# Kernel optimization log

Measured on AMD Instinct MI355X. Metric: run time of the kernel, lower is better.

Reference implementation:

```python
import jax, jax.numpy as jnp
import numpy as np

N_NODES = 50000
N_GRAPHS = 64
HID = 128
IN_DIM = 128
N_LAYERS = 3


def setup_inputs() -> dict:
    key = jax.random.key(0)
    ks = jax.random.split(key, 12)
    x = jax.random.normal(ks[0], (N_NODES, IN_DIM), dtype=jnp.float32)
    edge_index = jax.random.randint(ks[1], (2, 800000), 0, N_NODES, dtype=jnp.int64)
    batch = jnp.sort(jax.random.randint(ks[2], (N_NODES,), 0, N_GRAPHS, dtype=jnp.int64))
    s = 1.0 / np.sqrt(HID)
    W0 = jax.random.normal(ks[3], (IN_DIM, HID), dtype=jnp.float32) * s
    b0 = jnp.zeros((HID,), dtype=jnp.float32)
    Ws = jax.random.normal(ks[4], (N_LAYERS, HID, HID), dtype=jnp.float32) * s
    bs = jnp.zeros((N_LAYERS, HID), dtype=jnp.float32)
    W1 = jax.random.normal(ks[5], (HID, HID // 2), dtype=jnp.float32) * s
    b1 = jnp.zeros((HID // 2,), dtype=jnp.float32)
    W2 = jax.random.normal(ks[6], (HID // 2, 2), dtype=jnp.float32) * (1.0 / np.sqrt(HID // 2))
    b2 = jnp.zeros((2,), dtype=jnp.float32)
    return {"x": x, "edge_index": edge_index, "batch": batch,
            "W0": W0, "b0": b0, "Ws": Ws, "bs": bs,
            "W1": W1, "b1": b1, "W2": W2, "b2": b2}


def reference(x, edge_index, batch, W0, b0, Ws, bs, W1, b1, W2, b2):
    n = x.shape[0]
    # GCN: add self-loops, symmetric normalization D^-1/2 (A+I) D^-1/2
    loop = jnp.arange(n, dtype=edge_index.dtype)
    src = jnp.concatenate([edge_index[0], loop])  # [E+N]
    dst = jnp.concatenate([edge_index[1], loop])
    deg = jax.ops.segment_sum(jnp.ones_like(dst, dtype=x.dtype), dst, num_segments=n)
    dinv = jax.lax.rsqrt(jnp.maximum(deg, 1.0))
    coef = (dinv[src] * dinv[dst])[:, None]  # [E+N, 1]

    def gcn(h, W, b):
        hw = h @ W                                  # transform first (cheaper)
        agg = jax.ops.segment_sum(hw[src] * coef, dst, num_segments=n)
        return jax.nn.relu(agg + b)

    h = gcn(x, W0, b0)
    for i in range(Ws.shape[0]):
        h = gcn(h, Ws[i], bs[i])

    # global mean pool over graphs
    sums = jax.ops.segment_sum(h, batch, num_segments=N_GRAPHS)
    cnts = jax.ops.segment_sum(jnp.ones((n,), dtype=h.dtype), batch, num_segments=N_GRAPHS)
    pooled = sums / jnp.maximum(cnts, 1.0)[:, None]  # [G, HID]

    out = jax.nn.relu(pooled @ W1 + b1) @ W2 + b2    # [G, 2]
    return out
```

## Files before the change

kernel.cpp:

```cpp
#include <hip/hip_runtime.h>
#include <hip/hip_bf16.h>
#include <hip/hip_fp16.h>

#define HID 128
#define N_GRAPHS 64

__global__ void init_deg_kernel(int* __restrict__ deg, int n) {
    int i = blockIdx.x * 256 + threadIdx.x;
    if (i < n) deg[i] = 1;
}

__global__ void count_kernel(const int* __restrict__ dst, int* __restrict__ deg, int E) {
    int e = blockIdx.x * 256 + threadIdx.x;
    if (e < E) atomicAdd(&deg[dst[e]], 1);
}

__global__ __launch_bounds__(256) void scan_partial_kernel(const int* __restrict__ deg,
                                                           int* __restrict__ bsum, int n) {
    __shared__ int red[256];
    int t = threadIdx.x;
    int i = blockIdx.x * 256 + t;
    red[t] = (i < n) ? deg[i] : 0;
    __syncthreads();
#pragma unroll
    for (int s = 128; s > 0; s >>= 1) {
        if (t < s) red[t] += red[t + s];
        __syncthreads();
    }
    if (t == 0) bsum[blockIdx.x] = red[0];
}

__global__ __launch_bounds__(256) void scan_bsum_kernel(const int* __restrict__ bsum,
                                                        int* __restrict__ boff,
                                                        int* __restrict__ row_ptr,
                                                        int nb, int n) {
    __shared__ int arr[256];
    int t = threadIdx.x;
    int own = (t < nb) ? bsum[t] : 0;
    arr[t] = own;
    __syncthreads();
#pragma unroll
    for (int off = 1; off < 256; off <<= 1) {
        int v = arr[t];
        int add = (t >= off) ? arr[t - off] : 0;
        __syncthreads();
        arr[t] = v + add;
        __syncthreads();
    }
    if (t < nb) boff[t] = arr[t] - own;
    if (t == 255) row_ptr[n] = arr[255];
}

__global__ __launch_bounds__(256) void scan_emit_kernel(const int* __restrict__ deg,
                                                        const int* __restrict__ boff,
                                                        int* __restrict__ row_ptr,
                                                        int* __restrict__ cursor,
                                                        float* __restrict__ dinv, int n) {
    __shared__ int arr[256];
    int t = threadIdx.x;
    int i = blockIdx.x * 256 + t;
    int d = (i < n) ? deg[i] : 0;
    arr[t] = d;
    __syncthreads();
#pragma unroll
    for (int off = 1; off < 256; off <<= 1) {
        int v = arr[t];
        int add = (t >= off) ? arr[t - off] : 0;
        __syncthreads();
        arr[t] = v + add;
        __syncthreads();
    }
    if (i < n) {
        int pos = boff[blockIdx.x] + arr[t] - d;
        row_ptr[i] = pos;
        cursor[i] = pos;
        dinv[i] = rsqrtf((float)d);
    }
}

__global__ void fill_kernel(const int* __restrict__ src, const int* __restrict__ dst,
                            int* __restrict__ cursor, int* __restrict__ col,
                            int E, int EN) {
    int e = blockIdx.x * 256 + threadIdx.x;
    if (e >= EN) return;
    int s, d;
    if (e < E) { s = src[e]; d = dst[e]; }
    else       { s = e - E; d = s; }
    int pos = atomicAdd(&cursor[d], 1);
    col[pos] = s;
}

__global__ __launch_bounds__(256, 2) void gemm_scale_kernel(const float* __restrict__ A,
                                                            const float* __restrict__ W,
                                                            const float* __restrict__ dinv,
                                                            __half* __restrict__ out16, int M) {
    __shared__ float sAT[32][132];
    __shared__ float sW[32][132];
    int tid = threadIdx.x;
    int row0 = blockIdx.x * 128;
    int ty = tid >> 4, tx = tid & 15;
    int r0 = ty * 8;
    int cl = tx * 4;
    int ch = 64 + tx * 4;

    float acc[8][8];
#pragma unroll
    for (int i = 0; i < 8; ++i)
#pragma unroll
        for (int j = 0; j < 8; ++j) acc[i][j] = 0.f;

    for (int kc = 0; kc < 128; kc += 32) {
#pragma unroll
        for (int p = 0; p < 4; ++p) {
            int idx = tid + p * 256;
            int k = idx >> 5, c4 = idx & 31;
            float4 v = *(const float4*)(W + (size_t)(kc + k) * 128 + c4 * 4);
            *(float4*)&sW[k][c4 * 4] = v;
        }
#pragma unroll
        for (int p = 0; p < 4; ++p) {
            int idx = tid + p * 256;
            int r = idx >> 3, c4 = idx & 7;
            float4 v = make_float4(0.f, 0.f, 0.f, 0.f);
            if (row0 + r < M) v = *(const float4*)(A + (size_t)(row0 + r) * 128 + kc + c4 * 4);
            sAT[c4 * 4 + 0][r] = v.x;
            sAT[c4 * 4 + 1][r] = v.y;
            sAT[c4 * 4 + 2][r] = v.z;
            sAT[c4 * 4 + 3][r] = v.w;
        }
        __syncthreads();

#pragma unroll 4
        for (int k = 0; k < 32; ++k) {
            float4 a0 = *(float4*)&sAT[k][r0];
            float4 a1 = *(float4*)&sAT[k][r0 + 4];
            float4 w0 = *(float4*)&sW[k][cl];
            float4 w1 = *(float4*)&sW[k][ch];
            float a[8] = {a0.x, a0.y, a0.z, a0.w, a1.x, a1.y, a1.z, a1.w};
            float w[8] = {w0.x, w0.y, w0.z, w0.w, w1.x, w1.y, w1.z, w1.w};
#pragma unroll
            for (int i = 0; i < 8; ++i)
#pragma unroll
                for (int j = 0; j < 8; ++j)
                    acc[i][j] += a[i] * w[j];
        }
        __syncthreads();
    }

#pragma unroll
    for (int i = 0; i < 8; ++i) {
        int r = row0 + r0 + i;
        if (r < M) {
            float dv = dinv[r];
            __half2 h0 = __floats2half2_rn(acc[i][0] * dv, acc[i][1] * dv);
            __half2 h1 = __floats2half2_rn(acc[i][2] * dv, acc[i][3] * dv);
            __half2 h2 = __floats2half2_rn(acc[i][4] * dv, acc[i][5] * dv);
            __half2 h3 = __floats2half2_rn(acc[i][6] * dv, acc[i][7] * dv);
            float2 plo, phi;
            ((__half2*)&plo)[0] = h0; ((__half2*)&plo)[1] = h1;
            ((__half2*)&phi)[0] = h2; ((__half2*)&phi)[1] = h3;
            *(float2*)(out16 + (size_t)r * 128 + cl) = plo;
            *(float2*)(out16 + (size_t)r * 128 + ch) = phi;
        }
    }
}

__global__ __launch_bounds__(256) void aggregate_kernel(const __half* __restrict__ hw,
                                                        const int* __restrict__ row_ptr,
                                                        const int* __restrict__ col,
                                                        const float* __restrict__ dinv,
                                                        const float* __restrict__ bias,
                                                        float* __restrict__ out, int n) {
    int tid = threadIdx.x;
    int v = blockIdx.x * 8 + (tid >> 5);
    if (v >= n) return;
    int j = (tid & 31) * 4;
    int p0 = row_ptr[v], p1 = row_ptr[v + 1];
    float4 acc = make_float4(0.f, 0.f, 0.f, 0.f);
    int p = p0;
    for (; p + 3 < p1; p += 4) {
        int s0 = col[p], s1 = col[p + 1], s2 = col[p + 2], s3 = col[p + 3];
        float2 r0 = *(const float2*)(hw + (size_t)s0 * 128 + j);
        float2 r1 = *(const float2*)(hw + (size_t)s1 * 128 + j);
        float2 r2 = *(const float2*)(hw + (size_t)s2 * 128 + j);
        float2 r3 = *(const float2*)(hw + (size_t)s3 * 128 + j);
        float2 a0 = __half22float2(((__half2*)&r0)[0]), a1 = __half22float2(((__half2*)&r0)[1]);
        float2 b0 = __half22float2(((__half2*)&r1)[0]), b1 = __half22float2(((__half2*)&r1)[1]);
        float2 c0 = __half22float2(((__half2*)&r2)[0]), c1 = __half22float2(((__half2*)&r2)[1]);
        float2 d0 = __half22float2(((__half2*)&r3)[0]), d1 = __half22float2(((__half2*)&r3)[1]);
        acc.x += (a0.x + b0.x) + (c0.x + d0.x);
        acc.y += (a0.y + b0.y) + (c0.y + d0.y);
        acc.z += (a1.x + b1.x) + (c1.x + d1.x);
        acc.w += (a1.y + b1.y) + (c1.y + d1.y);
    }
    for (; p < p1; ++p) {
        int s0 = col[p];
        float2 r0 = *(const float2*)(hw + (size_t)s0 * 128 + j);
        float2 a0 = __half22float2(((__half2*)&r0)[0]), a1 = __half22float2(((__half2*)&r0)[1]);
        acc.x += a0.x; acc.y += a0.y; acc.z += a1.x; acc.w += a1.y;
    }
    float dv = dinv[v];
    float4 bb = *(const float4*)(bias + j);
    float4 o;
    o.x = fmaxf(acc.x * dv + bb.x, 0.f);
    o.y = fmaxf(acc.y * dv + bb.y, 0.f);
    o.z = fmaxf(acc.z * dv + bb.z, 0.f);
    o.w = fmaxf(acc.w * dv + bb.w, 0.f);
    *(float4*)(out + (size_t)v * 128 + j) = o;
}

__global__ void boundary_kernel(const int* __restrict__ batch, int* __restrict__ start, int n) {
    int i = blockIdx.x * 256 + threadIdx.x;
    if (i >= n) return;
    int b = batch[i];
    int pb = (i > 0) ? batch[i - 1] : -1;
    if (b != pb) {
        for (int g = pb + 1; g <= b; ++g) start[g] = i;
    }
    if (i == n - 1) {
        for (int g = b + 1; g <= N_GRAPHS; ++g) start[g] = n;
    }
}

__global__ __launch_bounds__(256) void pool_reduce_kernel(const float* __restrict__ h,
                                                          const int* __restrict__ start,
                                                          float* __restrict__ pooled) {
    __shared__ float part[8][128];
    int g = blockIdx.x;
    int s = start[g], e = start[g + 1];
    int tid = threadIdx.x;
    int grp = tid >> 5;
    int j = (tid & 31) * 4;
    float4 acc = make_float4(0.f, 0.f, 0.f, 0.f);
    for (int v = s + grp; v < e; v += 8) {
        float4 a = *(const float4*)(h + (size_t)v * 128 + j);
        acc.x += a.x; acc.y += a.y; acc.z += a.z; acc.w += a.w;
    }
    *(float4*)&part[grp][j] = acc;
    __syncthreads();
    if (tid < 128) {
        float sum = 0.f;
#pragma unroll
        for (int k = 0; k < 8; ++k) sum += part[k][tid];
        int cntv = e - s; if (cntv < 1) cntv = 1;
        pooled[g * 128 + tid] = sum / (float)cntv;
    }
}

__global__ __launch_bounds__(256) void mlp_kernel(const float* __restrict__ pooled_g,
                                                  const float* __restrict__ W1,
                                                  const float* __restrict__ b1,
                                                  const float* __restrict__ W2,
                                                  const float* __restrict__ b2,
                                                  float* __restrict__ out) {
    __shared__ float pooled[64][128];
    __shared__ float h1[64][64];
    int tid = threadIdx.x;
    for (int i = tid; i < 64 * 128; i += 256) pooled[i >> 7][i & 127] = pooled_g[i];
    __syncthreads();
    for (int i = tid; i < 64 * 64; i += 256) {
        int g = i >> 6, j = i & 63;
        float acc = b1[j];
        for (int k = 0; k < 128; ++k) acc += pooled[g][k] * W1[k * 64 + j];
        h1[g][j] = fmaxf(acc, 0.f);
    }
    __syncthreads();
    if (tid < 128) {
        int g = tid >> 1, c = tid & 1;
        float acc = b2[c];
        for (int jj = 0; jj < 64; ++jj) acc += h1[g][jj] * W2[jj * 2 + c];
        out[tid] = acc;
    }
}

extern "C" void kernel_launch(void* const* d_in, const int* in_sizes, int n_in,
                              void* d_out, int out_size, void* d_ws, size_t ws_size,
                              hipStream_t stream) {
    const float* x    = (const float*)d_in[0];
    const int*   ei   = (const int*)d_in[1];
    const int*   batch= (const int*)d_in[2];
    const float* W0   = (const float*)d_in[3];
    const float* b0   = (const float*)d_in[4];
    const float* Ws   = (const float*)d_in[5];
    const float* bs   = (const float*)d_in[6];
    const float* W1   = (const float*)d_in[7];
    const float* b1   = (const float*)d_in[8];
    const float* W2   = (const float*)d_in[9];
    const float* b2   = (const float*)d_in[10];
    float* out = (float*)d_out;

    const int n  = in_sizes[0] / HID;
    const int E  = in_sizes[1] / 2;
    const int EN = E + n;
    const int* src = ei;
    const int* dst = ei + E;
    const int nb = (n + 255) / 256;

    char* ws = (char*)d_ws;
    size_t off = 0;
    auto alloc = [&](size_t bytes) { void* p = ws + off; off = (off + bytes + 255) & ~(size_t)255; return p; };
    float*  bufA   = (float*) alloc((size_t)n * HID * 4);
    __half* hw16   = (__half*)alloc((size_t)n * HID * 2);
    float*  dinv   = (float*) alloc((size_t)n * 4);
    int*    row_ptr= (int*)   alloc((size_t)(n + 1) * 4);
    int*    cursor = (int*)   alloc((size_t)n * 4);
    int*    deg    = (int*)   alloc((size_t)n * 4);
    int*    col    = (int*)   alloc((size_t)EN * 4);
    int*    bsum   = (int*)   alloc((size_t)nb * 4);
    int*    boff   = (int*)   alloc((size_t)nb * 4);
    int*    gstart = (int*)   alloc((N_GRAPHS + 1) * 4);
    float*  pooled = (float*) alloc(N_GRAPHS * 128 * 4);
    (void)ws_size; (void)n_in; (void)out_size;

    init_deg_kernel<<<nb, 256, 0, stream>>>(deg, n);
    count_kernel<<<(E + 255) / 256, 256, 0, stream>>>(dst, deg, E);
    scan_partial_kernel<<<nb, 256, 0, stream>>>(deg, bsum, n);
    scan_bsum_kernel<<<1, 256, 0, stream>>>(bsum, boff, row_ptr, nb, n);
    scan_emit_kernel<<<nb, 256, 0, stream>>>(deg, boff, row_ptr, cursor, dinv, n);
    fill_kernel<<<(EN + 255) / 256, 256, 0, stream>>>(src, dst, cursor, col, E, EN);
    boundary_kernel<<<nb, 256, 0, stream>>>(batch, gstart, n);

    const int gemm_grid = (n + 127) / 128;
    const int node_grid = (n + 7) / 8;

    gemm_scale_kernel<<<gemm_grid, 256, 0, stream>>>(x, W0, dinv, hw16, n);
    aggregate_kernel<<<node_grid, 256, 0, stream>>>(hw16, row_ptr, col, dinv, b0, bufA, n);
    for (int l = 0; l < 3; ++l) {
        gemm_scale_kernel<<<gemm_grid, 256, 0, stream>>>(bufA, Ws + (size_t)l * HID * HID, dinv, hw16, n);
        aggregate_kernel<<<node_grid, 256, 0, stream>>>(hw16, row_ptr, col, dinv, bs + (size_t)l * HID, bufA, n);
    }

    pool_reduce_kernel<<<N_GRAPHS, 256, 0, stream>>>(bufA, gstart, pooled);
    mlp_kernel<<<1, 256, 0, stream>>>(pooled, W1, b1, W2, b2, out);
}
```

Before: 509.6 us.

## Double-buffer GEMM tiles with smaller row blocks and widen aggregate gathers

The GEMM now handles 64 rows per block instead of 128, with each thread computing an 8x4 tile. It double-buffers the A and W shared-memory tiles, loading the next K chunk into registers while the current chunk is being computed. This gives more blocks and hides global-load latency, but halves per-thread register reuse of the W values. The aggregate kernel now uses 16 threads per node, each gathering 16-byte (8 half) chunks, so each edge row is fetched with fewer, wider loads.

```diff
diff --git a/kernel.cpp b/kernel.cpp
--- a/kernel.cpp
+++ b/kernel.cpp
@@ -90,61 +90,98 @@
     col[pos] = s;
 }
 
-__global__ __launch_bounds__(256, 2) void gemm_scale_kernel(const float* __restrict__ A,
-                                                            const float* __restrict__ W,
-                                                            const float* __restrict__ dinv,
-                                                            __half* __restrict__ out16, int M) {
-    __shared__ float sAT[32][132];
-    __shared__ float sW[32][132];
+__global__ __launch_bounds__(256) void gemm_scale_kernel(const float* __restrict__ A,
+                                                         const float* __restrict__ W,
+                                                         const float* __restrict__ dinv,
+                                                         __half* __restrict__ out16, int M) {
+    __shared__ float sAT[2][32][68];
+    __shared__ float sW [2][32][132];
     int tid = threadIdx.x;
-    int row0 = blockIdx.x * 128;
-    int ty = tid >> 4, tx = tid & 15;
+    int row0 = blockIdx.x * 64;
+    int ty = tid >> 5, tx = tid & 31;
     int r0 = ty * 8;
-    int cl = tx * 4;
-    int ch = 64 + tx * 4;
-
-    float acc[8][8];
+    int j0 = tx * 4;
+
+    float acc[8][4];
 #pragma unroll
     for (int i = 0; i < 8; ++i)
 #pragma unroll
-        for (int j = 0; j < 8; ++j) acc[i][j] = 0.f;
-
-    for (int kc = 0; kc < 128; kc += 32) {
-#pragma unroll
-        for (int p = 0; p < 4; ++p) {
-            int idx = tid + p * 256;
-            int k = idx >> 5, c4 = idx & 31;
-            float4 v = *(const float4*)(W + (size_t)(kc + k) * 128 + c4 * 4);
-            *(float4*)&sW[k][c4 * 4] = v;
-        }
-#pragma unroll
-        for (int p = 0; p < 4; ++p) {
-            int idx = tid + p * 256;
-            int r = idx >> 3, c4 = idx & 7;
-            float4 v = make_float4(0.f, 0.f, 0.f, 0.f);
-            if (row0 + r < M) v = *(const float4*)(A + (size_t)(row0 + r) * 128 + kc + c4 * 4);
-            sAT[c4 * 4 + 0][r] = v.x;
-            sAT[c4 * 4 + 1][r] = v.y;
-            sAT[c4 * 4 + 2][r] = v.z;
-            sAT[c4 * 4 + 3][r] = v.w;
-        }
-        __syncthreads();
+        for (int j = 0; j < 4; ++j) acc[i][j] = 0.f;
+
+#pragma unroll
+    for (int p = 0; p < 4; ++p) {
+        int idx = tid + p * 256;
+        int k = idx >> 5, c4 = idx & 31;
+        *(float4*)&sW[0][k][c4 * 4] = *(const float4*)(W + (size_t)k * 128 + c4 * 4);
+    }
+#pragma unroll
+    for (int p = 0; p < 2; ++p) {
+        int idx = tid + p * 256;
+        int r = idx >> 3, c4 = idx & 7;
+        float4 v = make_float4(0.f, 0.f, 0.f, 0.f);
+        if (row0 + r < M) v = *(const float4*)(A + (size_t)(row0 + r) * 128 + c4 * 4);
+        sAT[0][c4 * 4 + 0][r] = v.x;
+        sAT[0][c4 * 4 + 1][r] = v.y;
+        sAT[0][c4 * 4 + 2][r] = v.z;
+        sAT[0][c4 * 4 + 3][r] = v.w;
+    }
+    __syncthreads();
+
+    for (int kci = 0; kci < 4; ++kci) {
+        int cur = kci & 1;
+        float4 wreg[4], areg[2];
+        if (kci < 3) {
+            int kc = (kci + 1) * 32;
+#pragma unroll
+            for (int p = 0; p < 4; ++p) {
+                int idx = tid + p * 256;
+                int k = idx >> 5, c4 = idx & 31;
+                wreg[p] = *(const float4*)(W + (size_t)(kc + k) * 128 + c4 * 4);
+            }
+#pragma unroll
+            for (int p = 0; p < 2; ++p) {
+                int idx = tid + p * 256;
+                int r = idx >> 3, c4 = idx & 7;
+                areg[p] = make_float4(0.f, 0.f, 0.f, 0.f);
+                if (row0 + r < M) areg[p] = *(const float4*)(A + (size_t)(row0 + r) * 128 + kc + c4 * 4);
+            }
+        }
 
 #pragma unroll 4
         for (int k = 0; k < 32; ++k) {
-            float4 a0 = *(float4*)&sAT[k][r0];
-            float4 a1 = *(float4*)&sAT[k][r0 + 4];
-            float4 w0 = *(float4*)&sW[k][cl];
-            float4 w1 = *(float4*)&sW[k][ch];
+            float4 a0 = *(float4*)&sAT[cur][k][r0];
+            float4 a1 = *(float4*)&sAT[cur][k][r0 + 4];
+            float4 w4 = *(float4*)&sW[cur][k][j0];
             float a[8] = {a0.x, a0.y, a0.z, a0.w, a1.x, a1.y, a1.z, a1.w};
-            float w[8] = {w0.x, w0.y, w0.z, w0.w, w1.x, w1.y, w1.z, w1.w};
-#pragma unroll
-            for (int i = 0; i < 8; ++i)
-#pragma unroll
-                for (int j = 0; j < 8; ++j)
-                    acc[i][j] += a[i] * w[j];
-        }
-        __syncthreads();
+#pragma unroll
+            for (int i = 0; i < 8; ++i) {
+                acc[i][0] += a[i] * w4.x;
+                acc[i][1] += a[i] * w4.y;
+                acc[i][2] += a[i] * w4.z;
+                acc[i][3] += a[i] * w4.w;
+            }
+        }
+        __syncthreads();
+
+        if (kci < 3) {
+            int nbuf = cur ^ 1;
+#pragma unroll
+            for (int p = 0; p < 4; ++p) {
+                int idx = tid + p * 256;
+                int k = idx >> 5, c4 = idx & 31;
+                *(float4*)&sW[nbuf][k][c4 * 4] = wreg[p];
+            }
+#pragma unroll
+            for (int p = 0; p < 2; ++p) {
+                int idx = tid + p * 256;
+                int r = idx >> 3, c4 = idx & 7;
+                sAT[nbuf][c4 * 4 + 0][r] = areg[p].x;
+                sAT[nbuf][c4 * 4 + 1][r] = areg[p].y;
+                sAT[nbuf][c4 * 4 + 2][r] = areg[p].z;
+                sAT[nbuf][c4 * 4 + 3][r] = areg[p].w;
+            }
+            __syncthreads();
+        }
     }
 
 #pragma unroll
@@ -154,13 +191,9 @@
             float dv = dinv[r];
             __half2 h0 = __floats2half2_rn(acc[i][0] * dv, acc[i][1] * dv);
             __half2 h1 = __floats2half2_rn(acc[i][2] * dv, acc[i][3] * dv);
-            __half2 h2 = __floats2half2_rn(acc[i][4] * dv, acc[i][5] * dv);
-            __half2 h3 = __floats2half2_rn(acc[i][6] * dv, acc[i][7] * dv);
-            float2 plo, phi;
-            ((__half2*)&plo)[0] = h0; ((__half2*)&plo)[1] = h1;
-            ((__half2*)&phi)[0] = h2; ((__half2*)&phi)[1] = h3;
-            *(float2*)(out16 + (size_t)r * 128 + cl) = plo;
-            *(float2*)(out16 + (size_t)r * 128 + ch) = phi;
+            float2 pk;
+            ((__half2*)&pk)[0] = h0; ((__half2*)&pk)[1] = h1;
+            *(float2*)(out16 + (size_t)r * 128 + j0) = pk;
         }
     }
 }
@@ -172,41 +205,60 @@
                                                         const float* __restrict__ bias,
                                                         float* __restrict__ out, int n) {
     int tid = threadIdx.x;
-    int v = blockIdx.x * 8 + (tid >> 5);
+    int v = blockIdx.x * 16 + (tid >> 4);
     if (v >= n) return;
-    int j = (tid & 31) * 4;
+    int j = (tid & 15) * 8;
     int p0 = row_ptr[v], p1 = row_ptr[v + 1];
-    float4 acc = make_float4(0.f, 0.f, 0.f, 0.f);
+    float acc[8];
+#pragma unroll
+    for (int q = 0; q < 8; ++q) acc[q] = 0.f;
+
     int p = p0;
     for (; p + 3 < p1; p += 4) {
         int s0 = col[p], s1 = col[p + 1], s2 = col[p + 2], s3 = col[p + 3];
-        float2 r0 = *(const float2*)(hw + (size_t)s0 * 128 + j);
-        float2 r1 = *(const float2*)(hw + (size_t)s1 * 128 + j);
-        float2 r2 = *(const float2*)(hw + (size_t)s2 * 128 + j);
-        float2 r3 = *(const float2*)(hw + (size_t)s3 * 128 + j);
-        float2 a0 = __half22float2(((__half2*)&r0)[0]), a1 = __half22float2(((__half2*)&r0)[1]);
-        float2 b0 = __half22float2(((__half2*)&r1)[0]), b1 = __half22float2(((__half2*)&r1)[1]);
-        float2 c0 = __half22float2(((__half2*)&r2)[0]), c1 = __half22float2(((__half2*)&r2)[1]);
-        float2 d0 = __half22float2(((__half2*)&r3)[0]), d1 = __half22float2(((__half2*)&r3)[1]);
-        acc.x += (a0.x + b0.x) + (c0.x + d0.x);
-        acc.y += (a0.y + b0.y) + (c0.y + d0.y);
-        acc.z += (a1.x + b1.x) + (c1.x + d1.x);
-        acc.w += (a1.y + b1.y) + (c1.y + d1.y);
+        float4 r0 = *(const float4*)(hw + (size_t)s0 * 128 + j);
+        float4 r1 = *(const float4*)(hw + (size_t)s1 * 128 + j);
+        float4 r2 = *(const float4*)(hw + (size_t)s2 * 128 + j);
+        float4 r3 = *(const float4*)(hw + (size_t)s3 * 128 + j);
+        const __half2* h0 = (const __half2*)&r0;
+        const __half2* h1 = (const __half2*)&r1;
+        const __half2* h2 = (const __half2*)&r2;
+        const __half2* h3 = (const __half2*)&r3;
+#pragma unroll
+        for (int q = 0; q < 4; ++q) {
+            float2 f0 = __half22float2(h0[q]);
+            float2 f1 = __half22float2(h1[q]);
+            float2 f2 = __half22float2(h2[q]);
+            float2 f3 = __half22float2(h3[q]);
+            acc[2 * q + 0] += (f0.x + f1.x) + (f2.x + f3.x);
+            acc[2 * q + 1] += (f0.y + f1.y) + (f2.y + f3.y);
+        }
     }
     for (; p < p1; ++p) {
         int s0 = col[p];
-        float2 r0 = *(const float2*)(hw + (size_t)s0 * 128 + j);
-        float2 a0 = __half22float2(((__half2*)&r0)[0]), a1 = __half22float2(((__half2*)&r0)[1]);
-        acc.x += a0.x; acc.y += a0.y; acc.z += a1.x; acc.w += a1.y;
+        float4 r0 = *(const float4*)(hw + (size_t)s0 * 128 + j);
+        const __half2* h0 = (const __half2*)&r0;
+#pragma unroll
+        for (int q = 0; q < 4; ++q) {
+            float2 f0 = __half22float2(h0[q]);
+            acc[2 * q + 0] += f0.x;
+            acc[2 * q + 1] += f0.y;
+        }
     }
     float dv = dinv[v];
-    float4 bb = *(const float4*)(bias + j);
-    float4 o;
-    o.x = fmaxf(acc.x * dv + bb.x, 0.f);
-    o.y = fmaxf(acc.y * dv + bb.y, 0.f);
-    o.z = fmaxf(acc.z * dv + bb.z, 0.f);
-    o.w = fmaxf(acc.w * dv + bb.w, 0.f);
-    *(float4*)(out + (size_t)v * 128 + j) = o;
+    float4 bb0 = *(const float4*)(bias + j);
+    float4 bb1 = *(const float4*)(bias + j + 4);
+    float4 o0, o1;
+    o0.x = fmaxf(acc[0] * dv + bb0.x, 0.f);
+    o0.y = fmaxf(acc[1] * dv + bb0.y, 0.f);
+    o0.z = fmaxf(acc[2] * dv + bb0.z, 0.f);
+    o0.w = fmaxf(acc[3] * dv + bb0.w, 0.f);
+    o1.x = fmaxf(acc[4] * dv + bb1.x, 0.f);
+    o1.y = fmaxf(acc[5] * dv + bb1.y, 0.f);
+    o1.z = fmaxf(acc[6] * dv + bb1.z, 0.f);
+    o1.w = fmaxf(acc[7] * dv + bb1.w, 0.f);
+    *(float4*)(out + (size_t)v * 128 + j) = o0;
+    *(float4*)(out + (size_t)v * 128 + j + 4) = o1;
 }
 
 __global__ void boundary_kernel(const int* __restrict__ batch, int* __restrict__ start, int n) {
@@ -320,8 +372,8 @@
     fill_kernel<<<(EN + 255) / 256, 256, 0, stream>>>(src, dst, cursor, col, E, EN);
     boundary_kernel<<<nb, 256, 0, stream>>>(batch, gstart, n);
 
-    const int gemm_grid = (n + 127) / 128;
-    const int node_grid = (n + 7) / 8;
+    const int gemm_grid = (n + 63) / 64;
+    const int node_grid = (n + 15) / 16;
 
     gemm_scale_kernel<<<gemm_grid, 256, 0, stream>>>(x, W0, dinv, hw16, n);
     aggregate_kernel<<<node_grid, 256, 0, stream>>>(hw16, row_ptr, col, dinv, b0, bufA, n);
```

Measured after the change: 511.0 us. No clear change (+0.3%).
